# Optimization experiments

Measured on AMD Instinct MI355X. Metric: run time of the kernel, lower is better.

Reference implementation:

```python
import jax, jax.numpy as jnp
import numpy as np
import math

D = 1024   # input dim
R = 256    # latent dim
K = 8192   # codebook size
N = 32768  # batch of vectors
BETA = 0.25


def setup_inputs() -> dict:
    key = jax.random.key(0)
    kx, kw, kc = jax.random.split(key, 3)
    x = jax.random.normal(kx, (N, D), dtype=jnp.float32)
    W = jax.random.normal(kw, (R, D), dtype=jnp.float32) / math.sqrt(D)
    code = jax.random.normal(kc, (K, R), dtype=jnp.float32) * 0.1
    return {"x": x, "W": W, "code": code}


def reference(x, W, code):
    # encode: z = x @ W^T  -> [N, R]
    z = jnp.einsum('nd,rd->nr', x, W)
    # pairwise squared distances to codebook: [N, K]
    d2 = (jnp.sum(z * z, axis=1, keepdims=True)
          + jnp.sum(code * code, axis=1)[None, :]
          - 2.0 * jnp.einsum('nr,kr->nk', z, code))
    idx = jnp.argmin(d2, axis=1)          # [N] int
    q = code[idx]                          # [N, R] gather
    # straight-through estimator
    zhat = z + jax.lax.stop_gradient(q - z)
    # decode: x_hat = zhat @ W  -> [N, D]
    x_hat = jnp.einsum('nr,rd->nd', zhat, W)
    rec = jnp.mean((x_hat - x) ** 2)
    codebook_loss = jnp.mean((q - jax.lax.stop_gradient(z)) ** 2)
    commit = jnp.mean((z - jax.lax.stop_gradient(q)) ** 2)
    loss = rec + codebook_loss + BETA * commit
    return (loss, rec, z, q, idx)
```

## Files before the change

kernel.cpp:

```cpp
#include <hip/hip_runtime.h>

#define NN 32768
#define DD 1024
#define RR 256
#define KK 8192

typedef float f32x4 __attribute__((ext_vector_type(4)));
typedef _Float16 half8 __attribute__((ext_vector_type(8)));
typedef _Float16 half4_t __attribute__((ext_vector_type(4)));

#define OFF_Z   2L
#define OFF_Q   (2L + (long)NN * RR)
#define OFF_IDX (2L + 2L * (long)NN * RR)

#define O_WT   0L
#define O_CF   524288L
#define O_CN   4718592L
#define O_A    4751360L
#define O_B    4882432L
#define O_M1   4915200L
#define O_KEY  5046272L
#define O_CNT  5308416L
#define O_FLAG 5308432L
#define O_LIST 5373952L
#define LIST_CAP 262144
#define FCAP 16384

#define TAU_S 0.025f

__global__ void k_wt(const float* __restrict__ W, _Float16* __restrict__ Wt) {
  __shared__ float tile[64][65];
  int d0 = blockIdx.x * 64, r0 = blockIdx.y * 64;
  int t = threadIdx.x;
#pragma unroll
  for (int it = 0; it < 16; ++it) {
    int i = t + it * 256;
    int r = i >> 6, d = i & 63;
    tile[r][d] = W[(long)(r0 + r) * DD + d0 + d];
  }
  __syncthreads();
#pragma unroll
  for (int it = 0; it < 16; ++it) {
    int i = t + it * 256;
    int d = i >> 6, r = i & 63;
    Wt[(long)(d0 + d) * RR + r0 + r] = (_Float16)tile[r][d];
  }
}

__global__ void k_code(const float* __restrict__ code, _Float16* __restrict__ cfs,
                       float* __restrict__ cnorm) {
  int k = blockIdx.x;
  int l = threadIdx.x;
  f32x4 v = ((const f32x4*)code)[(long)k * 64 + l];
  half4_t h;
#pragma unroll
  for (int j = 0; j < 4; ++j) h[j] = (_Float16)v[j];
  long dst = ((long)(k >> 4) << 12) + ((long)(l >> 3) << 9) +
             (((l >> 1) & 3) << 7) + ((k & 15) << 3) + ((l & 1) << 2);
  *(half4_t*)(cfs + dst) = h;
  float s = v[0]*v[0] + v[1]*v[1] + v[2]*v[2] + v[3]*v[3];
#pragma unroll
  for (int off = 1; off < 64; off <<= 1) s += __shfl_xor(s, off);
  if (l == 0) cnorm[k] = s;
}

__global__ __launch_bounds__(256, 3)
void k_npz(const float* __restrict__ x, const float* __restrict__ W,
           float* __restrict__ z) {
#pragma clang fp contract(off)
  __shared__ float wsl[128][65];
  __shared__ float xsl[32][64];
  int nb = blockIdx.x * 32;
  int rh = blockIdx.y * 128;
  int t = threadIdx.x;
  int rp = t & 63;
  int nh = t >> 6;
  f32x4 acc[8][2];
#pragma unroll
  for (int n = 0; n < 8; ++n)
#pragma unroll
    for (int q = 0; q < 2; ++q) acc[n][q] = (f32x4){0.f, 0.f, 0.f, 0.f};

  for (int ch = 0; ch < 16; ++ch) {
    __syncthreads();
#pragma unroll
    for (int it = 0; it < 8; ++it) {
      int idx = t + it * 256;
      int r = idx >> 4, kk = (idx & 15) << 2;
      *(f32x4*)&wsl[r][kk] = *(const f32x4*)(W + (long)(rh + r) * DD + ch * 64 + kk);
    }
#pragma unroll
    for (int it = 0; it < 2; ++it) {
      int idx = t + it * 256;
      int r = idx >> 4, kk = (idx & 15) << 2;
      *(f32x4*)&xsl[r][kk] = *(const f32x4*)(x + (long)(nb + r) * DD + ch * 64 + kk);
    }
    __syncthreads();
#pragma unroll 4
    for (int g = 0; g < 16; ++g) {
      f32x4 w0 = *(const f32x4*)&wsl[rp][g * 4];
      f32x4 w1 = *(const f32x4*)&wsl[rp + 64][g * 4];
#pragma unroll
      for (int n = 0; n < 8; ++n) {
        f32x4 xv = *(const f32x4*)&xsl[nh * 8 + n][g * 4];
        f32x4 p0 = xv * w0;
        acc[n][0] = acc[n][0] + p0;
        f32x4 p1 = xv * w1;
        acc[n][1] = acc[n][1] + p1;
      }
    }
  }
#pragma unroll
  for (int n = 0; n < 8; ++n)
#pragma unroll
    for (int q = 0; q < 2; ++q) {
      float sa = acc[n][q][0] + acc[n][q][1];
      float sb = acc[n][q][2] + acc[n][q][3];
      z[(long)(nb + nh * 8 + n) * RR + rh + rp + q * 64] = sa + sb;
    }
}

__device__ __forceinline__ float np_pw256_sq(const float* __restrict__ p) {
#pragma clang fp contract(off)
  float blk[2];
#pragma unroll
  for (int h = 0; h < 2; ++h) {
    const float* q = p + h * 128;
    float r[8];
#pragma unroll
    for (int j = 0; j < 8; ++j) { float v = q[j]; r[j] = v * v; }
    for (int i = 8; i < 128; i += 8) {
#pragma unroll
      for (int j = 0; j < 8; ++j) { float v = q[i + j]; r[j] = r[j] + v * v; }
    }
    float ta = r[0] + r[1], tb = r[2] + r[3], tc = r[4] + r[5], td = r[6] + r[7];
    blk[h] = (ta + tb) + (tc + td);
  }
  return blk[0] + blk[1];
}

__global__ void k_sumA(const float* __restrict__ z, float* __restrict__ A) {
  int n = blockIdx.x * 256 + threadIdx.x;
  A[n] = np_pw256_sq(z + (long)n * RR);
}

__global__ void k_sumB(const float* __restrict__ code, float* __restrict__ B) {
  int k = blockIdx.x * 256 + threadIdx.x;
  B[k] = np_pw256_sq(code + (long)k * RR);
}

__global__ __launch_bounds__(256, 2)
void k_argmin(const float* __restrict__ z, const _Float16* __restrict__ cfs,
              const float* __restrict__ cnorm, float* __restrict__ m1arr,
              float* __restrict__ idxf, int* __restrict__ flagcnt,
              int* __restrict__ flags, int fcap) {
  __shared__ float sm1[4][64], sm2[4][64], si1[4][64];
  int n0 = blockIdx.x * 64;
  int tid = threadIdx.x;
  int l = tid & 63, w = tid >> 6;
  int lr = l & 15, lg = l >> 4;

  half8 za[4][8];
#pragma unroll
  for (int rf = 0; rf < 4; ++rf) {
    const float* p = z + (long)(n0 + rf * 16 + lr) * RR + lg * 8;
#pragma unroll
    for (int ks = 0; ks < 8; ++ks) {
      f32x4 v0 = *(const f32x4*)(p + ks * 32);
      f32x4 v1 = *(const f32x4*)(p + ks * 32 + 4);
#pragma unroll
      for (int j = 0; j < 4; ++j) {
        za[rf][ks][j]     = (_Float16)v0[j];
        za[rf][ks][4 + j] = (_Float16)v1[j];
      }
    }
  }

  float m1[16], m2[16], i1[16];
#pragma unroll
  for (int s = 0; s < 16; ++s) { m1[s] = 3.4e38f; m2[s] = 3.4e38f; i1[s] = 0.f; }
  f32x4 zero = {0.f, 0.f, 0.f, 0.f};

  for (int ct = 0; ct < 128; ++ct) {
    int col0 = ct * 64 + w * 16;
    int c16 = ct * 4 + w;
    const _Float16* bp = cfs + ((long)c16 << 12) + (l << 3);
    float cn = cnorm[col0 + lr];
    float fi = (float)(col0 + lr);
    f32x4 a[4];
#pragma unroll
    for (int rf = 0; rf < 4; ++rf) a[rf] = zero;
#pragma unroll
    for (int ks = 0; ks < 8; ++ks) {
      half8 b = *(const half8*)(bp + ((long)ks << 9));
#pragma unroll
      for (int rf = 0; rf < 4; ++rf)
        a[rf] = __builtin_amdgcn_mfma_f32_16x16x32_f16(za[rf][ks], b, a[rf], 0, 0, 0);
    }
#pragma unroll
    for (int rf = 0; rf < 4; ++rf)
#pragma unroll
      for (int j = 0; j < 4; ++j) {
        int sl = rf * 4 + j;
        float s = fmaf(-2.f, a[rf][j], cn);
        float om1 = m1[sl];
        m2[sl] = fminf(m2[sl], fmaxf(s, om1));
        bool lt = s < om1;
        m1[sl] = lt ? s : om1;
        i1[sl] = lt ? fi : i1[sl];
      }
  }

#pragma unroll
  for (int sl = 0; sl < 16; ++sl) {
    float a1 = m1[sl], a2 = m2[sl], ai = i1[sl];
#pragma unroll
    for (int off = 1; off < 16; off <<= 1) {
      float b1 = __shfl_xor(a1, off);
      float b2 = __shfl_xor(a2, off);
      float bi = __shfl_xor(ai, off);
      float nm2 = fminf(fminf(a2, b2), fmaxf(a1, b1));
      bool take = (b1 < a1) || ((b1 == a1) && (bi < ai));
      a1 = take ? b1 : a1;
      ai = take ? bi : ai;
      a2 = nm2;
    }
    if (lr == 0) {
      int lrow = (sl >> 2) * 16 + lg * 4 + (sl & 3);
      sm1[w][lrow] = a1; sm2[w][lrow] = a2; si1[w][lrow] = ai;
    }
  }
  __syncthreads();
  if (tid < 64) {
    float a1 = sm1[0][tid], a2 = sm2[0][tid], ai = si1[0][tid];
#pragma unroll
    for (int ww = 1; ww < 4; ++ww) {
      float b1 = sm1[ww][tid], b2 = sm2[ww][tid], bi = si1[ww][tid];
      float nm2 = fminf(fminf(a2, b2), fmaxf(a1, b1));
      bool take = (b1 < a1) || ((b1 == a1) && (bi < ai));
      a1 = take ? b1 : a1;
      ai = take ? bi : ai;
      a2 = nm2;
    }
    int row = n0 + tid;
    idxf[row] = ai;
    m1arr[row] = a1;
    if (a2 - a1 < TAU_S) {
      int p = atomicAdd(flagcnt, 1);
      if (p < fcap) flags[p] = row;
    }
  }
}

__global__ __launch_bounds__(256, 2)
void k_collect(const float* __restrict__ z, const _Float16* __restrict__ cfs,
               const float* __restrict__ cnorm, const float* __restrict__ m1arr,
               const int* __restrict__ flagcnt, const int* __restrict__ flags,
               int fcap, int* __restrict__ listcnt, unsigned* __restrict__ list,
               int cap) {
  int n = *flagcnt; if (n > fcap) n = fcap;
  int n0 = blockIdx.x * 64;
  if (n0 >= n) return;
  int tid = threadIdx.x;
  int l = tid & 63, w = tid >> 6;
  int lr = l & 15, lg = l >> 4;

  half8 za[4][8];
#pragma unroll
  for (int rf = 0; rf < 4; ++rf) {
    int fidx = n0 + rf * 16 + lr;
    int zrow = (fidx < n) ? flags[fidx] : 0;
    const float* p = z + (long)zrow * RR + lg * 8;
#pragma unroll
    for (int ks = 0; ks < 8; ++ks) {
      f32x4 v0 = *(const f32x4*)(p + ks * 32);
      f32x4 v1 = *(const f32x4*)(p + ks * 32 + 4);
#pragma unroll
      for (int j = 0; j < 4; ++j) {
        za[rf][ks][j]     = (_Float16)v0[j];
        za[rf][ks][4 + j] = (_Float16)v1[j];
      }
    }
  }

  unsigned rows[16];
  float thr[16];
#pragma unroll
  for (int sl = 0; sl < 16; ++sl) {
    int fidx = n0 + (sl >> 2) * 16 + lg * 4 + (sl & 3);
    bool v = fidx < n;
    rows[sl] = v ? (unsigned)flags[fidx] : 0u;
    thr[sl] = v ? m1arr[rows[sl]] + TAU_S : -3.4e38f;
  }
  f32x4 zero = {0.f, 0.f, 0.f, 0.f};

  for (int ct = 0; ct < 128; ++ct) {
    int col0 = ct * 64 + w * 16;
    int c16 = ct * 4 + w;
    const _Float16* bp = cfs + ((long)c16 << 12) + (l << 3);
    float cn = cnorm[col0 + lr];
    unsigned cand = (unsigned)(col0 + lr);
    f32x4 a[4];
#pragma unroll
    for (int rf = 0; rf < 4; ++rf) a[rf] = zero;
#pragma unroll
    for (int ks = 0; ks < 8; ++ks) {
      half8 b = *(const half8*)(bp + ((long)ks << 9));
#pragma unroll
      for (int rf = 0; rf < 4; ++rf)
        a[rf] = __builtin_amdgcn_mfma_f32_16x16x32_f16(za[rf][ks], b, a[rf], 0, 0, 0);
    }
#pragma unroll
    for (int rf = 0; rf < 4; ++rf)
#pragma unroll
      for (int j = 0; j < 4; ++j) {
        int sl = rf * 4 + j;
        float s = fmaf(-2.f, a[rf][j], cn);
        if (s < thr[sl]) {
          int pos = atomicAdd(listcnt, 1);
          if (pos < cap) list[pos] = (rows[sl] << 13) | cand;
        }
      }
  }
}

__global__ void k_npd2(const float* __restrict__ z, const float* __restrict__ code,
                       const float* __restrict__ A, const float* __restrict__ B,
                       const int* __restrict__ listcnt, const unsigned* __restrict__ list,
                       unsigned long long* __restrict__ keys, int cap) {
#pragma clang fp contract(off)
  int n = *listcnt; if (n > cap) n = cap;
  for (int i = blockIdx.x * 256 + threadIdx.x; i < n; i += gridDim.x * 256) {
    unsigned e = list[i];
    int row = (int)(e >> 13), k = (int)(e & 8191u);
    const float* zp = z + (long)row * RR;
    const float* cp = code + (long)k * RR;
    float s0 = 0.f, s1 = 0.f, s2 = 0.f, s3 = 0.f;
    for (int g = 0; g < 64; ++g) {
      f32x4 zv = *(const f32x4*)(zp + g * 4);
      f32x4 cv = *(const f32x4*)(cp + g * 4);
      s0 = s0 + zv[0] * cv[0];
      s1 = s1 + zv[1] * cv[1];
      s2 = s2 + zv[2] * cv[2];
      s3 = s3 + zv[3] * cv[3];
    }
    float C = (s0 + s1) + (s2 + s3);
    float t1 = A[row] + B[k];
    float d2 = t1 - 2.0f * C;
    unsigned long long key = ((unsigned long long)__float_as_uint(d2) << 13) |
                             (unsigned long long)(unsigned)k;
    atomicMin(&keys[row], key);
  }
}

__global__ void k_fix(const int* __restrict__ flagcnt, const int* __restrict__ flags,
                      const unsigned long long* __restrict__ keys,
                      float* __restrict__ idxf, int fcap) {
  int n = *flagcnt; if (n > fcap) n = fcap;
  for (int i = blockIdx.x * 256 + threadIdx.x; i < n; i += gridDim.x * 256) {
    int row = flags[i];
    unsigned long long k = keys[row];
    if (k != ~0ULL) idxf[row] = (float)(unsigned)(k & 8191ULL);
  }
}

__global__ void k_gather(const float* __restrict__ code, const float* __restrict__ z,
                         const float* __restrict__ idxf, float* __restrict__ q,
                         float* __restrict__ cbsum) {
  int t = threadIdx.x;
  int rid = blockIdx.x * 4 + (t >> 6);
  int l = t & 63;
  int k = (int)idxf[rid];
  f32x4 cv = ((const f32x4*)code)[(long)k * 64 + l];
  f32x4 zv = ((const f32x4*)z)[(long)rid * 64 + l];
  ((f32x4*)q)[(long)rid * 64 + l] = cv;
  f32x4 d = cv - zv;
  float s = d[0]*d[0] + d[1]*d[1] + d[2]*d[2] + d[3]*d[3];
#pragma unroll
  for (int off = 1; off < 64; off <<= 1) s += __shfl_xor(s, off);
  __shared__ float sw[4];
  if (l == 0) sw[t >> 6] = s;
  __syncthreads();
  if (t == 0) atomicAdd(cbsum, sw[0] + sw[1] + sw[2] + sw[3]);
}

__global__ __launch_bounds__(512, 2)
void k_rec(const float* __restrict__ q, const _Float16* __restrict__ Wt,
           const float* __restrict__ x, float* __restrict__ recsum) {
  int n0 = blockIdx.x * 128;
  int d0 = blockIdx.y * 512;
  int tid = threadIdx.x;
  int l = tid & 63, w = tid >> 6;
  int wr = w >> 2, wc = w & 3;
  int lr = l & 15, lg = l >> 4;
  f32x4 zero = {0.f, 0.f, 0.f, 0.f};
  f32x4 acc[4][8];
#pragma unroll
  for (int a = 0; a < 4; ++a)
#pragma unroll
    for (int b = 0; b < 8; ++b) acc[a][b] = zero;

  for (int kk = 0; kk < 8; ++kk) {
    half8 aq[4];
#pragma unroll
    for (int rf = 0; rf < 4; ++rf) {
      const float* p = q + (long)(n0 + wr * 64 + rf * 16 + lr) * RR + kk * 32 + lg * 8;
      f32x4 v0 = *(const f32x4*)p;
      f32x4 v1 = *(const f32x4*)(p + 4);
#pragma unroll
      for (int j = 0; j < 4; ++j) {
        aq[rf][j]     = (_Float16)v0[j];
        aq[rf][4 + j] = (_Float16)v1[j];
      }
    }
#pragma unroll
    for (int cfg = 0; cfg < 8; ++cfg) {
      const _Float16* bp = Wt + (long)(d0 + wc * 128 + cfg * 16 + lr) * RR + kk * 32 + lg * 8;
      half8 b = *(const half8*)bp;
#pragma unroll
      for (int rf = 0; rf < 4; ++rf)
        acc[rf][cfg] = __builtin_amdgcn_mfma_f32_16x16x32_f16(aq[rf], b, acc[rf][cfg], 0, 0, 0);
    }
  }
  float s = 0.f;
#pragma unroll
  for (int rf = 0; rf < 4; ++rf)
#pragma unroll
    for (int cfg = 0; cfg < 8; ++cfg)
#pragma unroll
      for (int j = 0; j < 4; ++j) {
        int n = n0 + wr * 64 + rf * 16 + lg * 4 + j;
        int d = d0 + wc * 128 + cfg * 16 + lr;
        float df = acc[rf][cfg][j] - x[(long)n * DD + d];
        s = fmaf(df, df, s);
      }
#pragma unroll
  for (int off = 1; off < 64; off <<= 1) s += __shfl_xor(s, off);
  __shared__ float sw[8];
  if (l == 0) sw[w] = s;
  __syncthreads();
  if (tid == 0) {
    float t8 = 0.f;
#pragma unroll
    for (int i = 0; i < 8; ++i) t8 += sw[i];
    atomicAdd(recsum, t8);
  }
}

__global__ void k_final(const float* __restrict__ rs, const float* __restrict__ cbs,
                        float* __restrict__ out) {
  if (threadIdx.x == 0 && blockIdx.x == 0) {
    float rec = *rs * (1.0f / 33554432.0f);
    float cb  = *cbs * (1.0f / 8388608.0f);
    out[0] = rec + 1.25f * cb;
    out[1] = rec;
  }
}

extern "C" void kernel_launch(void* const* d_in, const int* in_sizes, int n_in,
                              void* d_out, int out_size, void* d_ws, size_t ws_size,
                              hipStream_t stream) {
  (void)in_sizes; (void)n_in; (void)out_size; (void)ws_size;
  const float* x    = (const float*)d_in[0];
  const float* W    = (const float*)d_in[1];
  const float* code = (const float*)d_in[2];
  float* out = (float*)d_out;
  char* ws = (char*)d_ws;

  _Float16* Wt = (_Float16*)(ws + O_WT);
  _Float16* cfs = (_Float16*)(ws + O_CF);
  float* cnorm = (float*)(ws + O_CN);
  float* A = (float*)(ws + O_A);
  float* B = (float*)(ws + O_B);
  float* m1arr = (float*)(ws + O_M1);
  unsigned long long* keys = (unsigned long long*)(ws + O_KEY);
  int* listcnt = (int*)(ws + O_CNT);
  int* flagcnt = (int*)(ws + O_CNT + 4);
  float* recsum = (float*)(ws + O_CNT + 8);
  float* cbsum  = (float*)(ws + O_CNT + 12);
  int* flags = (int*)(ws + O_FLAG);
  unsigned* list = (unsigned*)(ws + O_LIST);

  float* zp = out + OFF_Z;
  float* qp = out + OFF_Q;
  float* ip = out + OFF_IDX;

  hipMemsetAsync(ws + O_CNT, 0, 16, stream);
  hipMemsetAsync(ws + O_KEY, 0xFF, (size_t)NN * 8, stream);

  k_wt<<<dim3(16, 4), dim3(256), 0, stream>>>(W, Wt);
  k_code<<<dim3(KK), dim3(64), 0, stream>>>(code, cfs, cnorm);
  k_npz<<<dim3(1024, 2), dim3(256), 0, stream>>>(x, W, zp);
  k_sumA<<<dim3(128), dim3(256), 0, stream>>>(zp, A);
  k_sumB<<<dim3(32), dim3(256), 0, stream>>>(code, B);
  k_argmin<<<dim3(512), dim3(256), 0, stream>>>(zp, cfs, cnorm, m1arr, ip, flagcnt, flags, FCAP);
  k_collect<<<dim3(FCAP / 64), dim3(256), 0, stream>>>(zp, cfs, cnorm, m1arr, flagcnt, flags, FCAP, listcnt, list, LIST_CAP);
  k_npd2<<<dim3(256), dim3(256), 0, stream>>>(zp, code, A, B, listcnt, list, keys, LIST_CAP);
  k_fix<<<dim3(64), dim3(256), 0, stream>>>(flagcnt, flags, keys, ip, FCAP);
  k_gather<<<dim3(8192), dim3(256), 0, stream>>>(code, zp, ip, qp, cbsum);
  k_rec<<<dim3(256, 2), dim3(512), 0, stream>>>(qp, Wt, x, recsum);
  k_final<<<dim3(1), dim3(64), 0, stream>>>(recsum, cbsum, out);
}
```

Baseline: 1.009 ms.

## Drop LDS staging in z-encode GEMM, read pre-interleaved W directly from global

Adds a kernel that rewrites W into an interleaved float layout (groups of 4 along D, with R inner), so each thread in the encode kernel can load coalesced f32x4 weight vectors straight from global memory. The encode kernel no longer stages x and W tiles through shared memory with barriers, and reads x rows directly instead. Launch bounds drop from 3 to 2 blocks per CU to leave room for registers. The intent is to remove LDS traffic and synchronization, at the cost of relying on L1/L2 caching for reuse of x and W, plus one extra small preprocessing launch.

```diff
diff --git a/kernel.cpp b/kernel.cpp
--- a/kernel.cpp
+++ b/kernel.cpp
@@ -23,6 +23,7 @@
 #define O_CNT  5308416L
 #define O_FLAG 5308432L
 #define O_LIST 5373952L
+#define O_WQ   6422528L
 #define LIST_CAP 262144
 #define FCAP 16384
 
@@ -44,6 +45,26 @@
     int i = t + it * 256;
     int d = i >> 6, r = i & 63;
     Wt[(long)(d0 + d) * RR + r0 + r] = (_Float16)tile[r][d];
+  }
+}
+
+__global__ void k_wq(const float* __restrict__ W, float* __restrict__ Wq) {
+  __shared__ float tile[64][65];
+  int d0 = blockIdx.x * 64, r0 = blockIdx.y * 64;
+  int t = threadIdx.x;
+#pragma unroll
+  for (int it = 0; it < 16; ++it) {
+    int i = t + it * 256;
+    int r = i >> 6, d = i & 63;
+    tile[r][d] = W[(long)(r0 + r) * DD + d0 + d];
+  }
+  __syncthreads();
+#pragma unroll
+  for (int it = 0; it < 16; ++it) {
+    int i = t + it * 256;
+    int gg = i >> 8, rj = i & 255;
+    int rr = rj >> 2, j = rj & 3;
+    Wq[((long)(d0 / 4 + gg) * 256 + r0 + rr) * 4 + j] = tile[rr][gg * 4 + j];
   }
 }
 
@@ -64,50 +85,33 @@
   if (l == 0) cnorm[k] = s;
 }
 
-__global__ __launch_bounds__(256, 3)
-void k_npz(const float* __restrict__ x, const float* __restrict__ W,
+__global__ __launch_bounds__(256, 2)
+void k_npz(const float* __restrict__ x, const float* __restrict__ Wq,
            float* __restrict__ z) {
 #pragma clang fp contract(off)
-  __shared__ float wsl[128][65];
-  __shared__ float xsl[32][64];
   int nb = blockIdx.x * 32;
   int rh = blockIdx.y * 128;
   int t = threadIdx.x;
-  int rp = t & 63;
-  int nh = t >> 6;
+  int rp = t & 63, nh = t >> 6;
   f32x4 acc[8][2];
 #pragma unroll
-  for (int n = 0; n < 8; ++n)
-#pragma unroll
-    for (int q = 0; q < 2; ++q) acc[n][q] = (f32x4){0.f, 0.f, 0.f, 0.f};
-
-  for (int ch = 0; ch < 16; ++ch) {
-    __syncthreads();
-#pragma unroll
-    for (int it = 0; it < 8; ++it) {
-      int idx = t + it * 256;
-      int r = idx >> 4, kk = (idx & 15) << 2;
-      *(f32x4*)&wsl[r][kk] = *(const f32x4*)(W + (long)(rh + r) * DD + ch * 64 + kk);
-    }
-#pragma unroll
-    for (int it = 0; it < 2; ++it) {
-      int idx = t + it * 256;
-      int r = idx >> 4, kk = (idx & 15) << 2;
-      *(f32x4*)&xsl[r][kk] = *(const f32x4*)(x + (long)(nb + r) * DD + ch * 64 + kk);
-    }
-    __syncthreads();
-#pragma unroll 4
-    for (int g = 0; g < 16; ++g) {
-      f32x4 w0 = *(const f32x4*)&wsl[rp][g * 4];
-      f32x4 w1 = *(const f32x4*)&wsl[rp + 64][g * 4];
-#pragma unroll
-      for (int n = 0; n < 8; ++n) {
-        f32x4 xv = *(const f32x4*)&xsl[nh * 8 + n][g * 4];
-        f32x4 p0 = xv * w0;
-        acc[n][0] = acc[n][0] + p0;
-        f32x4 p1 = xv * w1;
-        acc[n][1] = acc[n][1] + p1;
-      }
+  for (int n = 0; n < 8; ++n) {
+    acc[n][0] = (f32x4){0.f, 0.f, 0.f, 0.f};
+    acc[n][1] = (f32x4){0.f, 0.f, 0.f, 0.f};
+  }
+  const f32x4* wq = (const f32x4*)Wq + rh + rp;
+  const float* xr = x + (long)(nb + nh * 8) * DD;
+#pragma unroll 2
+  for (int g = 0; g < 256; ++g) {
+    f32x4 w0 = wq[(long)g * 256];
+    f32x4 w1 = wq[(long)g * 256 + 64];
+#pragma unroll
+    for (int n = 0; n < 8; ++n) {
+      f32x4 xv = *(const f32x4*)(xr + (long)n * DD + g * 4);
+      f32x4 p0 = xv * w0;
+      acc[n][0] = acc[n][0] + p0;
+      f32x4 p1 = xv * w1;
+      acc[n][1] = acc[n][1] + p1;
     }
   }
 #pragma unroll
@@ -480,6 +484,7 @@
   float* cbsum  = (float*)(ws + O_CNT + 12);
   int* flags = (int*)(ws + O_FLAG);
   unsigned* list = (unsigned*)(ws + O_LIST);
+  float* Wq = (float*)(ws + O_WQ);
 
   float* zp = out + OFF_Z;
   float* qp = out + OFF_Q;
@@ -489,8 +494,9 @@
   hipMemsetAsync(ws + O_KEY, 0xFF, (size_t)NN * 8, stream);
 
   k_wt<<<dim3(16, 4), dim3(256), 0, stream>>>(W, Wt);
+  k_wq<<<dim3(16, 4), dim3(256), 0, stream>>>(W, Wq);
   k_code<<<dim3(KK), dim3(64), 0, stream>>>(code, cfs, cnorm);
-  k_npz<<<dim3(1024, 2), dim3(256), 0, stream>>>(x, W, zp);
+  k_npz<<<dim3(1024, 2), dim3(256), 0, stream>>>(x, Wq, zp);
   k_sumA<<<dim3(128), dim3(256), 0, stream>>>(zp, A);
   k_sumB<<<dim3(32), dim3(256), 0, stream>>>(code, B);
   k_argmin<<<dim3(512), dim3(256), 0, stream>>>(zp, cfs, cnorm, m1arr, ip, flagcnt, flags, FCAP);
```

Result: slower. 1.362 ms (+35.0%).
